# Performance work log

Hardware: AMD Instinct MI355X
Metric: run time of the kernel (lower is better)

Reference implementation:

```python
import jax, jax.numpy as jnp
import numpy as np

TOPK = 8
N_EXPERTS = 64
ROUTE_SCALE = 1.0


def setup_inputs() -> dict:
    key = jax.random.key(0)
    k1, k2 = jax.random.split(key)
    x = jax.random.normal(k1, (16, 256, 64, 64), dtype=jnp.float32)
    gate_w = jax.random.normal(k2, (64, 256, 3, 3), dtype=jnp.float32) * 0.02  # [E, C, kh, kw]
    bias = jnp.zeros((64,), dtype=jnp.float32)  # load-balancing bias buffer
    return {"x": x, "gate_w": gate_w, "bias": bias}


def reference(x, gate_w, bias):
    # 3x3 conv, stride 1, pad 1 (SAME), no conv bias -> expert logits [B, E, H, W]
    logits = jax.lax.conv_general_dilated(
        x, gate_w, window_strides=(1, 1), padding="SAME",
        dimension_numbers=("NCHW", "OIHW", "NCHW"))
    scores = jax.nn.sigmoid(logits)                 # [B, E, H, W]
    s = jnp.moveaxis(scores, 1, -1)                 # [B, H, W, E]
    biased = s + bias                               # bias broadcast over experts
    _, idx = jax.lax.top_k(biased, TOPK)            # [B, H, W, K] (topk on biased scores)
    w = jnp.take_along_axis(s, idx, axis=-1)        # gather UNbiased scores
    w = jax.nn.softmax(w, axis=-1) * ROUTE_SCALE    # softmax over the K selected experts
    weights = jnp.moveaxis(w, -1, 1)                # [B, K, H, W] to match torch layout
    indices = jnp.moveaxis(idx, -1, 1)              # [B, K, H, W]
    counts = jnp.zeros((N_EXPERTS,), jnp.int32).at[idx.ravel()].add(1)  # bincount
    return weights, indices, counts
```

## Files before the change

kernel.cpp:

```cpp
#include <hip/hip_runtime.h>


typedef _Float16 half8 __attribute__((ext_vector_type(8)));
typedef __attribute__((ext_vector_type(4))) float f32x4;

#define LOG2E 1.44269504f

__device__ __forceinline__ unsigned short f2h_bits(float f) {
    _Float16 h = (_Float16)f;
    unsigned short b;
    __builtin_memcpy(&b, &h, 2);
    return b;
}

constexpr int WB_U4 = 8 * 9 * 4 * 64;

__global__ __launch_bounds__(256) void gate_prep(const float* __restrict__ gw,
                                                 unsigned short* __restrict__ wB) {
    int g = blockIdx.x * 256 + threadIdx.x;
    if (g >= WB_U4) return;
    int lane = g & 63;
    int nt   = (g >> 6) & 3;
    int rest = g >> 8;
    int t = rest % 9, q = rest / 9;
    int e  = nt * 16 + (lane & 15);
    int c0 = q * 32 + (lane >> 4) * 8;
    unsigned short o[8];
#pragma unroll
    for (int j = 0; j < 8; ++j)
        o[j] = f2h_bits(gw[(e * 256 + c0 + j) * 9 + t]);
    uint4 pk;
    pk.x = (unsigned)o[0] | ((unsigned)o[1] << 16);
    pk.y = (unsigned)o[2] | ((unsigned)o[3] << 16);
    pk.z = (unsigned)o[4] | ((unsigned)o[5] << 16);
    pk.w = (unsigned)o[6] | ((unsigned)o[7] << 16);
    ((uint4*)wB)[g] = pk;
}

constexpr int CSTR  = 40;
constexpr int XROW  = 66 * CSTR;
constexpr int XSBUF = 4 * XROW;
constexpr int SSTR  = 68;

__global__ __launch_bounds__(256, 2) void gate_main(
    const float* __restrict__ x, const float* __restrict__ bias,
    const unsigned short* __restrict__ wB, float* __restrict__ out) {
    __shared__ unsigned short xs[2 * XSBUF];
    __shared__ uint4 bbuf[2304];
    __shared__ float bias_s[64];
    __shared__ int   hist[64];

    const int tid  = threadIdx.x;
    const int lane = tid & 63;
    const int rw   = tid >> 6;
    const int blk  = blockIdx.x;
    const int b    = blk & 15;
    const int rp   = blk >> 4;

    if (tid < 64) { bias_s[tid] = bias[tid]; hist[tid] = 0; }

    const int r0  = tid >> 6;
    const int ws_ = tid & 63;
    const int gr  = rp * 2 - 1 + r0;
    const bool rok = (gr >= 0 && gr < 64);

    float va[32];
    uint4 vB[9];

    auto load_x = [&](int q) {
        const float* p0 = x + (((b * 256 + q * 32) * 64 + gr) * 64 + ws_);
        if (rok) {
#pragma unroll
            for (int u = 0; u < 32; ++u) va[u] = p0[u * 4096];
        } else {
#pragma unroll
            for (int u = 0; u < 32; ++u) va[u] = 0.f;
        }
    };
    auto store_x = [&](unsigned short* dst) {
        unsigned short* d0 = dst + (r0 * 66 + (ws_ + 1)) * CSTR;
#pragma unroll
        for (int c8 = 0; c8 < 4; ++c8) {
            uint4 pk;
            pk.x = (unsigned)f2h_bits(va[c8*8+0]) | ((unsigned)f2h_bits(va[c8*8+1]) << 16);
            pk.y = (unsigned)f2h_bits(va[c8*8+2]) | ((unsigned)f2h_bits(va[c8*8+3]) << 16);
            pk.z = (unsigned)f2h_bits(va[c8*8+4]) | ((unsigned)f2h_bits(va[c8*8+5]) << 16);
            pk.w = (unsigned)f2h_bits(va[c8*8+6]) | ((unsigned)f2h_bits(va[c8*8+7]) << 16);
            *(uint4*)(d0 + c8 * 8) = pk;
        }
        if (tid < 32) {
            int hr = tid >> 3, hc = (tid >> 2) & 1, hg = tid & 3;
            uint4 z = {0, 0, 0, 0};
            *(uint4*)(dst + (hr * 66 + hc * 65) * CSTR + hg * 8) = z;
        }
    };
    auto load_B = [&](int q) {
        const uint4* src = (const uint4*)wB + q * 2304 + tid;
#pragma unroll
        for (int k = 0; k < 9; ++k) vB[k] = src[k * 256];
    };
    auto store_B = [&]() {
#pragma unroll
        for (int k = 0; k < 9; ++k) bbuf[tid + k * 256] = vB[k];
    };

    f32x4 acc[2][4];
#pragma unroll
    for (int mt = 0; mt < 2; ++mt)
#pragma unroll
        for (int nt = 0; nt < 4; ++nt) acc[mt][nt] = (f32x4){0.f, 0.f, 0.f, 0.f};

    const int half_ = rw & 1, rloc = rw >> 1;

    auto compute = [&](const unsigned short* buf) {
#pragma unroll
        for (int t = 0; t < 9; ++t) {
            const int kh = t / 3, kw = t % 3;
            const unsigned short* abase =
                buf + ((rloc + kh) * 66 + half_ * 32 + kw + (lane & 15)) * CSTR +
                (lane >> 4) * 8;
            half8 afr[2];
#pragma unroll
            for (int mt = 0; mt < 2; ++mt)
                afr[mt] = *(const half8*)(abase + mt * 16 * CSTR);
            const uint4* bp = bbuf + t * 4 * 64 + lane;
#pragma unroll
            for (int nt = 0; nt < 4; ++nt) {
                half8 bfr = *(const half8*)(bp + nt * 64);
#pragma unroll
                for (int mt = 0; mt < 2; ++mt)
                    acc[mt][nt] = __builtin_amdgcn_mfma_f32_16x16x32_f16(
                        afr[mt], bfr, acc[mt][nt], 0, 0, 0);
            }
        }
    };

    load_x(0);
    load_B(0);
    store_x(xs);
    store_B();
    __syncthreads();
#pragma unroll 1
    for (int q = 0; q < 8; ++q) {
        const unsigned short* cur = xs + (q & 1) * XSBUF;
        if (q < 7) {
            load_x(q + 1);
            load_B(q + 1);
            compute(cur);
            store_x(xs + ((q + 1) & 1) * XSBUF);
            __syncthreads();
            store_B();
            __syncthreads();
        } else {
            compute(cur);
            __syncthreads();
        }
    }

    float* scf = (float*)xs;
#pragma unroll
    for (int mt = 0; mt < 2; ++mt)
#pragma unroll
        for (int nt = 0; nt < 4; ++nt)
#pragma unroll
            for (int rr = 0; rr < 4; ++rr) {
                float v = acc[mt][nt][rr];
                float s = 1.f / (1.f + __builtin_amdgcn_exp2f(-v * LOG2E));
                int m16 = ((lane >> 4) << 2) + rr;
                int p   = rloc * 64 + half_ * 32 + mt * 16 + m16;
                int e   = nt * 16 + (lane & 15);
                scf[p * SSTR + e] = s;
            }
    __syncthreads();

    if (tid < 128) {
        const float* row = scf + tid * SSTR;
        float tv[8];
        int   ti[8];
#pragma unroll
        for (int k = 0; k < 8; ++k) { tv[k] = -3.0e38f; ti[k] = 0; }
#pragma unroll
        for (int j4 = 0; j4 < 16; ++j4) {
            f32x4 blkv = *(const f32x4*)(row + j4 * 4);
#pragma unroll
            for (int j = 0; j < 4; ++j) {
                int   e  = j4 * 4 + j;
                float bs = blkv[j] + bias_s[e];
                if (bs > tv[7]) {
                    tv[7] = bs; ti[7] = e;
#pragma unroll
                    for (int k = 7; k > 0; --k) {
                        float fa = tv[k - 1], fb = tv[k];
                        int   ia = ti[k - 1], ib = ti[k];
                        bool  sw = fb > fa;
                        tv[k - 1] = sw ? fb : fa; tv[k] = sw ? fa : fb;
                        ti[k - 1] = sw ? ib : ia; ti[k] = sw ? ia : ib;
                    }
                }
            }
        }
        float u[8], mx = -3.0e38f;
#pragma unroll
        for (int k = 0; k < 8; ++k) { u[k] = tv[k] - bias_s[ti[k]]; mx = fmaxf(mx, u[k]); }
        float ex[8], sum = 0.f;
#pragma unroll
        for (int k = 0; k < 8; ++k) { ex[k] = __builtin_amdgcn_exp2f((u[k] - mx) * LOG2E); sum += ex[k]; }
        float inv = 1.f / sum;

        int h = rp * 2 + (tid >> 6), w = tid & 63;
        int obase = b * 32768 + h * 64 + w;
#pragma unroll
        for (int k = 0; k < 8; ++k) {
            out[obase + k * 4096]          = ex[k] * inv;
            out[524288 + obase + k * 4096] = (float)ti[k];
            atomicAdd(&hist[ti[k]], 1);
        }
    }
    __syncthreads();
    if (tid < 64) atomicAdd(out + 1048576 + tid, (float)hist[tid]);
}

extern "C" void kernel_launch(void* const* d_in, const int* in_sizes, int n_in,
                              void* d_out, int out_size, void* d_ws, size_t ws_size,
                              hipStream_t stream) {
    const float* x    = (const float*)d_in[0];
    const float* gw   = (const float*)d_in[1];
    const float* bias = (const float*)d_in[2];
    float* out = (float*)d_out;
    unsigned short* wB = (unsigned short*)d_ws;

    hipMemsetAsync((char*)d_out + (size_t)1048576 * sizeof(float), 0,
                   64 * sizeof(float), stream);
    gate_prep<<<72, 256, 0, stream>>>(gw, wB);
    gate_main<<<512, 256, 0, stream>>>(x, bias, wB, out);
}
```

Baseline: 173.0 us.

## Shrink tile to one output row per block, load weights to registers, drop double buffering

Each block now computes one output row (64 pixels) instead of two. The four waves split pixels and experts 2x2, and the grid doubles to 1024 blocks with a launch bound allowing 4 blocks per CU. Weight fragments are read from global memory straight into registers, so the shared-memory weight buffer and the double-buffered input staging are gone. LDS shrinks to a single input slab that is reused for the score matrix. The aim is higher occupancy so that other resident blocks hide latency, at the cost of twice the halo-row reloads and an unpipelined load-then-compute loop with two barriers per channel chunk.

```diff
diff --git a/kernel.cpp b/kernel.cpp
--- a/kernel.cpp
+++ b/kernel.cpp
@@ -38,142 +38,125 @@
 }
 
 constexpr int CSTR  = 40;
-constexpr int XROW  = 66 * CSTR;
-constexpr int XSBUF = 4 * XROW;
 constexpr int SSTR  = 68;
-
-__global__ __launch_bounds__(256, 2) void gate_main(
+constexpr int SCF_B = 64 * SSTR * 4;
+
+__global__ __launch_bounds__(256, 4) void gate_main(
     const float* __restrict__ x, const float* __restrict__ bias,
     const unsigned short* __restrict__ wB, float* __restrict__ out) {
-    __shared__ unsigned short xs[2 * XSBUF];
-    __shared__ uint4 bbuf[2304];
-    __shared__ float bias_s[64];
-    __shared__ int   hist[64];
+    __shared__ unsigned char smem[SCF_B + 512];
+    unsigned short* xs     = (unsigned short*)smem;
+    float*          scf    = (float*)smem;
+    float*          bias_s = (float*)(smem + SCF_B);
+    int*            hist   = (int*)(smem + SCF_B + 256);
 
     const int tid  = threadIdx.x;
     const int lane = tid & 63;
     const int rw   = tid >> 6;
     const int blk  = blockIdx.x;
     const int b    = blk & 15;
-    const int rp   = blk >> 4;
+    const int r    = blk >> 4;
 
     if (tid < 64) { bias_s[tid] = bias[tid]; hist[tid] = 0; }
 
-    const int r0  = tid >> 6;
-    const int ws_ = tid & 63;
-    const int gr  = rp * 2 - 1 + r0;
-    const bool rok = (gr >= 0 && gr < 64);
-
-    float va[32];
-    uint4 vB[9];
-
-    auto load_x = [&](int q) {
-        const float* p0 = x + (((b * 256 + q * 32) * 64 + gr) * 64 + ws_);
-        if (rok) {
-#pragma unroll
-            for (int u = 0; u < 32; ++u) va[u] = p0[u * 4096];
-        } else {
-#pragma unroll
-            for (int u = 0; u < 32; ++u) va[u] = 0.f;
+    const int  r0   = tid >> 6;
+    const int  w_   = tid & 63;
+    const bool smain = (tid < 192);
+    const int  gr   = r - 1 + r0;
+    const bool rok  = smain && (gr >= 0) && (gr < 64);
+    const float* xbase = x + (((size_t)(b * 256) * 64 + gr) * 64 + w_);
+    unsigned short* sdst = xs + (r0 * 66 + (w_ + 1)) * CSTR;
+
+    auto stage = [&](int q) {
+        if (smain) {
+            const float* p = xbase + (size_t)q * 32 * 4096;
+            if (rok) {
+#pragma unroll
+                for (int bt = 0; bt < 4; ++bt) {
+                    float v0 = p[(bt*8+0)*4096], v1 = p[(bt*8+1)*4096];
+                    float v2 = p[(bt*8+2)*4096], v3 = p[(bt*8+3)*4096];
+                    float v4 = p[(bt*8+4)*4096], v5 = p[(bt*8+5)*4096];
+                    float v6 = p[(bt*8+6)*4096], v7 = p[(bt*8+7)*4096];
+                    uint4 pk;
+                    pk.x = (unsigned)f2h_bits(v0) | ((unsigned)f2h_bits(v1) << 16);
+                    pk.y = (unsigned)f2h_bits(v2) | ((unsigned)f2h_bits(v3) << 16);
+                    pk.z = (unsigned)f2h_bits(v4) | ((unsigned)f2h_bits(v5) << 16);
+                    pk.w = (unsigned)f2h_bits(v6) | ((unsigned)f2h_bits(v7) << 16);
+                    *(uint4*)(sdst + bt * 8) = pk;
+                }
+            } else {
+                uint4 z = {0, 0, 0, 0};
+#pragma unroll
+                for (int bt = 0; bt < 4; ++bt) *(uint4*)(sdst + bt * 8) = z;
+            }
+        } else if (tid < 192 + 24) {
+            int idx = tid - 192;
+            int hr = idx >> 3, hc = (idx >> 2) & 1, hg = idx & 3;
+            uint4 z = {0, 0, 0, 0};
+            *(uint4*)(xs + (hr * 66 + hc * 65) * CSTR + hg * 8) = z;
         }
     };
-    auto store_x = [&](unsigned short* dst) {
-        unsigned short* d0 = dst + (r0 * 66 + (ws_ + 1)) * CSTR;
-#pragma unroll
-        for (int c8 = 0; c8 < 4; ++c8) {
-            uint4 pk;
-            pk.x = (unsigned)f2h_bits(va[c8*8+0]) | ((unsigned)f2h_bits(va[c8*8+1]) << 16);
-            pk.y = (unsigned)f2h_bits(va[c8*8+2]) | ((unsigned)f2h_bits(va[c8*8+3]) << 16);
-            pk.z = (unsigned)f2h_bits(va[c8*8+4]) | ((unsigned)f2h_bits(va[c8*8+5]) << 16);
-            pk.w = (unsigned)f2h_bits(va[c8*8+6]) | ((unsigned)f2h_bits(va[c8*8+7]) << 16);
-            *(uint4*)(d0 + c8 * 8) = pk;
-        }
-        if (tid < 32) {
-            int hr = tid >> 3, hc = (tid >> 2) & 1, hg = tid & 3;
-            uint4 z = {0, 0, 0, 0};
-            *(uint4*)(dst + (hr * 66 + hc * 65) * CSTR + hg * 8) = z;
-        }
-    };
-    auto load_B = [&](int q) {
-        const uint4* src = (const uint4*)wB + q * 2304 + tid;
-#pragma unroll
-        for (int k = 0; k < 9; ++k) vB[k] = src[k * 256];
-    };
-    auto store_B = [&]() {
-#pragma unroll
-        for (int k = 0; k < 9; ++k) bbuf[tid + k * 256] = vB[k];
-    };
-
-    f32x4 acc[2][4];
+
+    const int ph = rw >> 1;
+    const int eh = rw & 1;
+
+    f32x4 acc[2][2];
 #pragma unroll
     for (int mt = 0; mt < 2; ++mt)
 #pragma unroll
-        for (int nt = 0; nt < 4; ++nt) acc[mt][nt] = (f32x4){0.f, 0.f, 0.f, 0.f};
-
-    const int half_ = rw & 1, rloc = rw >> 1;
-
-    auto compute = [&](const unsigned short* buf) {
+        for (int nt = 0; nt < 2; ++nt) acc[mt][nt] = (f32x4){0.f, 0.f, 0.f, 0.f};
+
+#pragma unroll 1
+    for (int q = 0; q < 8; ++q) {
+        uint4 Bf[18];
+#pragma unroll
+        for (int t = 0; t < 9; ++t)
+#pragma unroll
+            for (int ntl = 0; ntl < 2; ++ntl)
+                Bf[t * 2 + ntl] = ((const uint4*)wB)
+                    [((q * 9 + t) * 4 + eh * 2 + ntl) * 64 + lane];
+
+        __syncthreads();
+        stage(q);
+        __syncthreads();
+
 #pragma unroll
         for (int t = 0; t < 9; ++t) {
             const int kh = t / 3, kw = t % 3;
             const unsigned short* abase =
-                buf + ((rloc + kh) * 66 + half_ * 32 + kw + (lane & 15)) * CSTR +
-                (lane >> 4) * 8;
+                xs + (kh * 66 + kw + ph * 32 + (lane & 15)) * CSTR + (lane >> 4) * 8;
             half8 afr[2];
 #pragma unroll
             for (int mt = 0; mt < 2; ++mt)
                 afr[mt] = *(const half8*)(abase + mt * 16 * CSTR);
-            const uint4* bp = bbuf + t * 4 * 64 + lane;
-#pragma unroll
-            for (int nt = 0; nt < 4; ++nt) {
-                half8 bfr = *(const half8*)(bp + nt * 64);
+#pragma unroll
+            for (int ntl = 0; ntl < 2; ++ntl) {
+                half8 bfr;
+                __builtin_memcpy(&bfr, &Bf[t * 2 + ntl], 16);
 #pragma unroll
                 for (int mt = 0; mt < 2; ++mt)
-                    acc[mt][nt] = __builtin_amdgcn_mfma_f32_16x16x32_f16(
-                        afr[mt], bfr, acc[mt][nt], 0, 0, 0);
-            }
-        }
-    };
-
-    load_x(0);
-    load_B(0);
-    store_x(xs);
-    store_B();
+                    acc[mt][ntl] = __builtin_amdgcn_mfma_f32_16x16x32_f16(
+                        afr[mt], bfr, acc[mt][ntl], 0, 0, 0);
+            }
+        }
+    }
+
     __syncthreads();
-#pragma unroll 1
-    for (int q = 0; q < 8; ++q) {
-        const unsigned short* cur = xs + (q & 1) * XSBUF;
-        if (q < 7) {
-            load_x(q + 1);
-            load_B(q + 1);
-            compute(cur);
-            store_x(xs + ((q + 1) & 1) * XSBUF);
-            __syncthreads();
-            store_B();
-            __syncthreads();
-        } else {
-            compute(cur);
-            __syncthreads();
-        }
-    }
-
-    float* scf = (float*)xs;
 #pragma unroll
     for (int mt = 0; mt < 2; ++mt)
 #pragma unroll
-        for (int nt = 0; nt < 4; ++nt)
+        for (int nt = 0; nt < 2; ++nt)
 #pragma unroll
             for (int rr = 0; rr < 4; ++rr) {
                 float v = acc[mt][nt][rr];
                 float s = 1.f / (1.f + __builtin_amdgcn_exp2f(-v * LOG2E));
-                int m16 = ((lane >> 4) << 2) + rr;
-                int p   = rloc * 64 + half_ * 32 + mt * 16 + m16;
-                int e   = nt * 16 + (lane & 15);
+                int p = ph * 32 + mt * 16 + ((lane >> 4) << 2) + rr;
+                int e = eh * 32 + nt * 16 + (lane & 15);
                 scf[p * SSTR + e] = s;
             }
     __syncthreads();
 
-    if (tid < 128) {
+    if (tid < 64) {
         const float* row = scf + tid * SSTR;
         float tv[8];
         int   ti[8];
@@ -207,8 +190,7 @@
         for (int k = 0; k < 8; ++k) { ex[k] = __builtin_amdgcn_exp2f((u[k] - mx) * LOG2E); sum += ex[k]; }
         float inv = 1.f / sum;
 
-        int h = rp * 2 + (tid >> 6), w = tid & 63;
-        int obase = b * 32768 + h * 64 + w;
+        int obase = b * 32768 + r * 64 + tid;
 #pragma unroll
         for (int k = 0; k < 8; ++k) {
             out[obase + k * 4096]          = ex[k] * inv;
@@ -232,5 +214,5 @@
     hipMemsetAsync((char*)d_out + (size_t)1048576 * sizeof(float), 0,
                    64 * sizeof(float), stream);
     gate_prep<<<72, 256, 0, stream>>>(gw, wB);
-    gate_main<<<512, 256, 0, stream>>>(x, bias, wB, out);
-}
+    gate_main<<<1024, 256, 0, stream>>>(x, bias, wB, out);
+}
```

New measurement: 167.3 us. -3.3%, faster.

## Restructure gate conv to single-wavefront blocks with register-pipelined tap prefetch

Applied to the files above, without the earlier changes.

Each block is now one 64-lane wavefront that computes one output row (64 pixels × 64 experts) instead of four waves covering two rows. Weights are read straight from global into registers with a three-slot prefetch ring instead of being staged in LDS. Loading and committing the next input channel chunk is interleaved tap by tap with the MFMAs, and with no cross-wave sharing all __syncthreads barriers are removed. The cost is that each block loads a 3-row halo for only one output row, so x is read about three times instead of twice. Weights are also read from global once per block, and per-wave register pressure is higher.

```diff
diff --git a/kernel.cpp b/kernel.cpp
--- a/kernel.cpp
+++ b/kernel.cpp
@@ -37,187 +37,200 @@
     ((uint4*)wB)[g] = pk;
 }
 
-constexpr int CSTR  = 40;
-constexpr int XROW  = 66 * CSTR;
-constexpr int XSBUF = 4 * XROW;
-constexpr int SSTR  = 68;
-
-__global__ __launch_bounds__(256, 2) void gate_main(
+constexpr int CSTR = 40;
+constexpr int SLAB = 3 * 66 * CSTR;
+constexpr int SSTR = 68;
+
+__global__ __launch_bounds__(64, 2) void gate_main(
     const float* __restrict__ x, const float* __restrict__ bias,
     const unsigned short* __restrict__ wB, float* __restrict__ out) {
-    __shared__ unsigned short xs[2 * XSBUF];
-    __shared__ uint4 bbuf[2304];
+    __shared__ unsigned short xs[2 * SLAB];
     __shared__ float bias_s[64];
     __shared__ int   hist[64];
 
-    const int tid  = threadIdx.x;
-    const int lane = tid & 63;
-    const int rw   = tid >> 6;
+    const int lane = threadIdx.x;
     const int blk  = blockIdx.x;
     const int b    = blk & 15;
-    const int rp   = blk >> 4;
-
-    if (tid < 64) { bias_s[tid] = bias[tid]; hist[tid] = 0; }
-
-    const int r0  = tid >> 6;
-    const int ws_ = tid & 63;
-    const int gr  = rp * 2 - 1 + r0;
-    const bool rok = (gr >= 0 && gr < 64);
-
-    float va[32];
-    uint4 vB[9];
-
-    auto load_x = [&](int q) {
-        const float* p0 = x + (((b * 256 + q * 32) * 64 + gr) * 64 + ws_);
-        if (rok) {
-#pragma unroll
-            for (int u = 0; u < 32; ++u) va[u] = p0[u * 4096];
-        } else {
-#pragma unroll
-            for (int u = 0; u < 32; ++u) va[u] = 0.f;
-        }
-    };
-    auto store_x = [&](unsigned short* dst) {
-        unsigned short* d0 = dst + (r0 * 66 + (ws_ + 1)) * CSTR;
-#pragma unroll
-        for (int c8 = 0; c8 < 4; ++c8) {
-            uint4 pk;
-            pk.x = (unsigned)f2h_bits(va[c8*8+0]) | ((unsigned)f2h_bits(va[c8*8+1]) << 16);
-            pk.y = (unsigned)f2h_bits(va[c8*8+2]) | ((unsigned)f2h_bits(va[c8*8+3]) << 16);
-            pk.z = (unsigned)f2h_bits(va[c8*8+4]) | ((unsigned)f2h_bits(va[c8*8+5]) << 16);
-            pk.w = (unsigned)f2h_bits(va[c8*8+6]) | ((unsigned)f2h_bits(va[c8*8+7]) << 16);
-            *(uint4*)(d0 + c8 * 8) = pk;
-        }
-        if (tid < 32) {
-            int hr = tid >> 3, hc = (tid >> 2) & 1, hg = tid & 3;
-            uint4 z = {0, 0, 0, 0};
-            *(uint4*)(dst + (hr * 66 + hc * 65) * CSTR + hg * 8) = z;
-        }
-    };
-    auto load_B = [&](int q) {
-        const uint4* src = (const uint4*)wB + q * 2304 + tid;
-#pragma unroll
-        for (int k = 0; k < 9; ++k) vB[k] = src[k * 256];
-    };
-    auto store_B = [&]() {
-#pragma unroll
-        for (int k = 0; k < 9; ++k) bbuf[tid + k * 256] = vB[k];
-    };
-
-    f32x4 acc[2][4];
-#pragma unroll
-    for (int mt = 0; mt < 2; ++mt)
+    const int r    = blk >> 4;
+
+    bias_s[lane] = bias[lane];
+    hist[lane]   = 0;
+
+    auto issue = [&](int qn, int p, float* tb) {
+        const int si = p >> 1, chh = p & 1;
+        const int s  = lane + si * 64;
+        if (s < 198) {
+            const int row = s / 66, wp = s - row * 66;
+            const int gr = r - 1 + row, gw = wp - 1;
+            if (gr >= 0 && gr < 64 && gw >= 0 && gw < 64) {
+                const float* p0 =
+                    x + (((size_t)(b * 256 + qn * 32 + chh * 16) * 64 + gr) * 64 + gw);
+#pragma unroll
+                for (int u = 0; u < 16; ++u) tb[u] = p0[(size_t)u * 4096];
+            } else {
+#pragma unroll
+                for (int u = 0; u < 16; ++u) tb[u] = 0.f;
+            }
+        }
+    };
+    auto commit = [&](int p, const float* tb, unsigned short* dst) {
+        const int si = p >> 1, chh = p & 1;
+        const int s  = lane + si * 64;
+        if (s < 198) {
+            const int row = s / 66, wp = s - row * 66;
+            unsigned short* d = dst + (row * 66 + wp) * CSTR + chh * 16;
+#pragma unroll
+            for (int h8 = 0; h8 < 2; ++h8) {
+                uint4 pk;
+                pk.x = (unsigned)f2h_bits(tb[h8*8+0]) | ((unsigned)f2h_bits(tb[h8*8+1]) << 16);
+                pk.y = (unsigned)f2h_bits(tb[h8*8+2]) | ((unsigned)f2h_bits(tb[h8*8+3]) << 16);
+                pk.z = (unsigned)f2h_bits(tb[h8*8+4]) | ((unsigned)f2h_bits(tb[h8*8+5]) << 16);
+                pk.w = (unsigned)f2h_bits(tb[h8*8+6]) | ((unsigned)f2h_bits(tb[h8*8+7]) << 16);
+                *(uint4*)(d + h8 * 8) = pk;
+            }
+        }
+    };
+
+    half8 Aa[3][4];
+    uint4 Bb[3][4];
+    auto prefA = [&](const unsigned short* buf, int t, int slot) {
+        const int kh = t / 3, kw = t % 3;
+#pragma unroll
+        for (int mt = 0; mt < 4; ++mt)
+            Aa[slot][mt] = *(const half8*)(
+                buf + (kh * 66 + mt * 16 + (lane & 15) + kw) * CSTR + (lane >> 4) * 8);
+    };
+    auto prefB = [&](int q_, int t_, int slot) {
+        const uint4* bp = (const uint4*)wB + ((q_ * 9 + t_) * 4) * 64 + lane;
+#pragma unroll
+        for (int nt = 0; nt < 4; ++nt) Bb[slot][nt] = bp[nt * 64];
+    };
+
+    f32x4 acc[4][4];
+#pragma unroll
+    for (int mt = 0; mt < 4; ++mt)
 #pragma unroll
         for (int nt = 0; nt < 4; ++nt) acc[mt][nt] = (f32x4){0.f, 0.f, 0.f, 0.f};
 
-    const int half_ = rw & 1, rloc = rw >> 1;
-
-    auto compute = [&](const unsigned short* buf) {
-#pragma unroll
-        for (int t = 0; t < 9; ++t) {
-            const int kh = t / 3, kw = t % 3;
-            const unsigned short* abase =
-                buf + ((rloc + kh) * 66 + half_ * 32 + kw + (lane & 15)) * CSTR +
-                (lane >> 4) * 8;
-            half8 afr[2];
-#pragma unroll
-            for (int mt = 0; mt < 2; ++mt)
-                afr[mt] = *(const half8*)(abase + mt * 16 * CSTR);
-            const uint4* bp = bbuf + t * 4 * 64 + lane;
-#pragma unroll
-            for (int nt = 0; nt < 4; ++nt) {
-                half8 bfr = *(const half8*)(bp + nt * 64);
-#pragma unroll
-                for (int mt = 0; mt < 2; ++mt)
-                    acc[mt][nt] = __builtin_amdgcn_mfma_f32_16x16x32_f16(
-                        afr[mt], bfr, acc[mt][nt], 0, 0, 0);
-            }
-        }
-    };
-
-    load_x(0);
-    load_B(0);
-    store_x(xs);
-    store_B();
-    __syncthreads();
+    auto mfma_tap = [&](int t) {
+        const int slot = t % 3;
+#pragma unroll
+        for (int nt = 0; nt < 4; ++nt) {
+            half8 bfr;
+            __builtin_memcpy(&bfr, &Bb[slot][nt], 16);
+#pragma unroll
+            for (int mt = 0; mt < 4; ++mt)
+                acc[mt][nt] = __builtin_amdgcn_mfma_f32_16x16x32_f16(
+                    Aa[slot][mt], bfr, acc[mt][nt], 0, 0, 0);
+        }
+    };
+
+    float t0b[16], t1b[16];
+
+    issue(0, 0, t0b); issue(0, 1, t1b);
+    commit(0, t0b, xs); issue(0, 2, t0b);
+    commit(1, t1b, xs); issue(0, 3, t1b);
+    commit(2, t0b, xs); issue(0, 4, t0b);
+    commit(3, t1b, xs); issue(0, 5, t1b);
+    commit(4, t0b, xs); issue(0, 6, t0b);
+    commit(5, t1b, xs); issue(0, 7, t1b);
+    commit(6, t0b, xs);
+    commit(7, t1b, xs);
+    prefA(xs, 0, 0);
+    prefB(0, 0, 0);
+
 #pragma unroll 1
     for (int q = 0; q < 8; ++q) {
-        const unsigned short* cur = xs + (q & 1) * XSBUF;
+        const unsigned short* cur = xs + (q & 1) * SLAB;
+        unsigned short*       nxt = xs + ((q + 1) & 1) * SLAB;
         if (q < 7) {
-            load_x(q + 1);
-            load_B(q + 1);
-            compute(cur);
-            store_x(xs + ((q + 1) & 1) * XSBUF);
-            __syncthreads();
-            store_B();
-            __syncthreads();
+            issue(q + 1, 0, t0b); issue(q + 1, 1, t1b);
+            prefA(cur, 1, 1); prefB(q, 1, 1); mfma_tap(0);
+            prefA(cur, 2, 2); prefB(q, 2, 2); mfma_tap(1);
+            commit(0, t0b, nxt); issue(q + 1, 2, t0b);
+            prefA(cur, 3, 0); prefB(q, 3, 0); mfma_tap(2);
+            commit(1, t1b, nxt); issue(q + 1, 3, t1b);
+            prefA(cur, 4, 1); prefB(q, 4, 1); mfma_tap(3);
+            commit(2, t0b, nxt); issue(q + 1, 4, t0b);
+            prefA(cur, 5, 2); prefB(q, 5, 2); mfma_tap(4);
+            commit(3, t1b, nxt); issue(q + 1, 5, t1b);
+            prefA(cur, 6, 0); prefB(q, 6, 0); mfma_tap(5);
+            commit(4, t0b, nxt); issue(q + 1, 6, t0b);
+            prefA(cur, 7, 1); prefB(q, 7, 1); mfma_tap(6);
+            commit(5, t1b, nxt); issue(q + 1, 7, t1b);
+            prefA(cur, 8, 2); prefB(q, 8, 2); mfma_tap(7);
+            commit(6, t0b, nxt);
+            commit(7, t1b, nxt);
+            prefA(nxt, 0, 0); prefB(q + 1, 0, 0);
+            mfma_tap(8);
         } else {
-            compute(cur);
-            __syncthreads();
+            prefA(cur, 1, 1); prefB(q, 1, 1); mfma_tap(0);
+            prefA(cur, 2, 2); prefB(q, 2, 2); mfma_tap(1);
+            prefA(cur, 3, 0); prefB(q, 3, 0); mfma_tap(2);
+            prefA(cur, 4, 1); prefB(q, 4, 1); mfma_tap(3);
+            prefA(cur, 5, 2); prefB(q, 5, 2); mfma_tap(4);
+            prefA(cur, 6, 0); prefB(q, 6, 0); mfma_tap(5);
+            prefA(cur, 7, 1); prefB(q, 7, 1); mfma_tap(6);
+            prefA(cur, 8, 2); prefB(q, 8, 2); mfma_tap(7);
+            mfma_tap(8);
         }
     }
 
     float* scf = (float*)xs;
 #pragma unroll
-    for (int mt = 0; mt < 2; ++mt)
+    for (int mt = 0; mt < 4; ++mt)
 #pragma unroll
         for (int nt = 0; nt < 4; ++nt)
 #pragma unroll
             for (int rr = 0; rr < 4; ++rr) {
                 float v = acc[mt][nt][rr];
                 float s = 1.f / (1.f + __builtin_amdgcn_exp2f(-v * LOG2E));
-                int m16 = ((lane >> 4) << 2) + rr;
-                int p   = rloc * 64 + half_ * 32 + mt * 16 + m16;
-                int e   = nt * 16 + (lane & 15);
+                int p = mt * 16 + ((lane >> 4) << 2) + rr;
+                int e = nt * 16 + (lane & 15);
                 scf[p * SSTR + e] = s;
             }
-    __syncthreads();
-
-    if (tid < 128) {
-        const float* row = scf + tid * SSTR;
-        float tv[8];
-        int   ti[8];
-#pragma unroll
-        for (int k = 0; k < 8; ++k) { tv[k] = -3.0e38f; ti[k] = 0; }
-#pragma unroll
-        for (int j4 = 0; j4 < 16; ++j4) {
-            f32x4 blkv = *(const f32x4*)(row + j4 * 4);
-#pragma unroll
-            for (int j = 0; j < 4; ++j) {
-                int   e  = j4 * 4 + j;
-                float bs = blkv[j] + bias_s[e];
-                if (bs > tv[7]) {
-                    tv[7] = bs; ti[7] = e;
-#pragma unroll
-                    for (int k = 7; k > 0; --k) {
-                        float fa = tv[k - 1], fb = tv[k];
-                        int   ia = ti[k - 1], ib = ti[k];
-                        bool  sw = fb > fa;
-                        tv[k - 1] = sw ? fb : fa; tv[k] = sw ? fa : fb;
-                        ti[k - 1] = sw ? ib : ia; ti[k] = sw ? ia : ib;
-                    }
+
+    const float* row = scf + lane * SSTR;
+    float tv[8];
+    int   ti[8];
+#pragma unroll
+    for (int k = 0; k < 8; ++k) { tv[k] = -3.0e38f; ti[k] = 0; }
+#pragma unroll
+    for (int j4 = 0; j4 < 16; ++j4) {
+        f32x4 blkv = *(const f32x4*)(row + j4 * 4);
+#pragma unroll
+        for (int j = 0; j < 4; ++j) {
+            int   e  = j4 * 4 + j;
+            float bs = blkv[j] + bias_s[e];
+            if (bs > tv[7]) {
+                tv[7] = bs; ti[7] = e;
+#pragma unroll
+                for (int k = 7; k > 0; --k) {
+                    float fa = tv[k - 1], fb = tv[k];
+                    int   ia = ti[k - 1], ib = ti[k];
+                    bool  sw = fb > fa;
+                    tv[k - 1] = sw ? fb : fa; tv[k] = sw ? fa : fb;
+                    ti[k - 1] = sw ? ib : ia; ti[k] = sw ? ia : ib;
                 }
             }
         }
-        float u[8], mx = -3.0e38f;
-#pragma unroll
-        for (int k = 0; k < 8; ++k) { u[k] = tv[k] - bias_s[ti[k]]; mx = fmaxf(mx, u[k]); }
-        float ex[8], sum = 0.f;
-#pragma unroll
-        for (int k = 0; k < 8; ++k) { ex[k] = __builtin_amdgcn_exp2f((u[k] - mx) * LOG2E); sum += ex[k]; }
-        float inv = 1.f / sum;
-
-        int h = rp * 2 + (tid >> 6), w = tid & 63;
-        int obase = b * 32768 + h * 64 + w;
-#pragma unroll
-        for (int k = 0; k < 8; ++k) {
-            out[obase + k * 4096]          = ex[k] * inv;
-            out[524288 + obase + k * 4096] = (float)ti[k];
-            atomicAdd(&hist[ti[k]], 1);
-        }
     }
-    __syncthreads();
-    if (tid < 64) atomicAdd(out + 1048576 + tid, (float)hist[tid]);
+    float u[8], mx = -3.0e38f;
+#pragma unroll
+    for (int k = 0; k < 8; ++k) { u[k] = tv[k] - bias_s[ti[k]]; mx = fmaxf(mx, u[k]); }
+    float ex[8], sum = 0.f;
+#pragma unroll
+    for (int k = 0; k < 8; ++k) { ex[k] = __builtin_amdgcn_exp2f((u[k] - mx) * LOG2E); sum += ex[k]; }
+    float inv = 1.f / sum;
+
+    const int obase = b * 32768 + r * 64 + lane;
+#pragma unroll
+    for (int k = 0; k < 8; ++k) {
+        out[obase + k * 4096]          = ex[k] * inv;
+        out[524288 + obase + k * 4096] = (float)ti[k];
+        atomicAdd(&hist[ti[k]], 1);
+    }
+    atomicAdd(out + 1048576 + lane, (float)hist[lane]);
 }
 
 extern "C" void kernel_launch(void* const* d_in, const int* in_sizes, int n_in,
@@ -232,5 +245,5 @@
     hipMemsetAsync((char*)d_out + (size_t)1048576 * sizeof(float), 0,
                    64 * sizeof(float), stream);
     gate_prep<<<72, 256, 0, stream>>>(gw, wB);
-    gate_main<<<512, 256, 0, stream>>>(x, bias, wB, out);
-}
+    gate_main<<<1024, 64, 0, stream>>>(x, bias, wB, out);
+}
```

After: 195.7 us. 1.13x slower.
